# Optimization experiments

Hardware: AMD Instinct MI355X
Metric: run time of the kernel (lower is better)

## Reference

```python
import jax, jax.numpy as jnp
import numpy as np
from jax.scipy.special import logsumexp

V, E, H, T, L = 100000, 300, 512, 24, 4096


def _lstm_dir(x, w_ih, w_hh, b, reverse):
    # x: [L, Din] -> hs: [L, H]; PyTorch gate order i, f, g, o
    if reverse:
        x = x[::-1]
    pre = x @ w_ih.T + b  # [L, 4H], input projection hoisted out of scan

    def step(carry, zt):
        h, c = carry
        z = zt + h @ w_hh.T
        i, f, g, o = jnp.split(z, 4)
        i, f, o = jax.nn.sigmoid(i), jax.nn.sigmoid(f), jax.nn.sigmoid(o)
        c = f * c + i * jnp.tanh(g)
        h = o * jnp.tanh(c)
        return (h, c), h

    z0 = (jnp.zeros(H, x.dtype), jnp.zeros(H, x.dtype))
    _, hs = jax.lax.scan(step, z0, pre)
    if reverse:
        hs = hs[::-1]
    return hs


def _crf_nll(emissions, tags, start_trans, end_trans, trans):
    # emissions: [L, T], tags: [L] int. Returns -log p(tags | emissions).
    n = emissions.shape[0]
    num = (start_trans[tags[0]]
           + emissions[jnp.arange(n), tags].sum()
           + trans[tags[:-1], tags[1:]].sum()
           + end_trans[tags[-1]])

    def step(alpha, e_t):
        alpha = logsumexp(alpha[:, None] + trans, axis=0) + e_t
        return alpha, None

    alpha0 = start_trans + emissions[0]
    alpha, _ = jax.lax.scan(step, alpha0, emissions[1:])
    den = logsumexp(alpha + end_trans)
    return den - num


def setup_inputs() -> dict:
    key = jax.random.key(0)
    ks = jax.random.split(key, 24)
    s = 0.05
    inp = {
        'emb': jax.random.normal(ks[0], (V, E), jnp.float32),
        'w_ih_l0f': s * jax.random.normal(ks[1], (4 * H, E), jnp.float32),
        'w_hh_l0f': s * jax.random.normal(ks[2], (4 * H, H), jnp.float32),
        'b_l0f': s * jax.random.normal(ks[3], (4 * H,), jnp.float32),
        'w_ih_l0b': s * jax.random.normal(ks[4], (4 * H, E), jnp.float32),
        'w_hh_l0b': s * jax.random.normal(ks[5], (4 * H, H), jnp.float32),
        'b_l0b': s * jax.random.normal(ks[6], (4 * H,), jnp.float32),
        'w_ih_l1f': s * jax.random.normal(ks[7], (4 * H, 2 * H), jnp.float32),
        'w_hh_l1f': s * jax.random.normal(ks[8], (4 * H, H), jnp.float32),
        'b_l1f': s * jax.random.normal(ks[9], (4 * H,), jnp.float32),
        'w_ih_l1b': s * jax.random.normal(ks[10], (4 * H, 2 * H), jnp.float32),
        'w_hh_l1b': s * jax.random.normal(ks[11], (4 * H, H), jnp.float32),
        'b_l1b': s * jax.random.normal(ks[12], (4 * H,), jnp.float32),
        'w_out': s * jax.random.normal(ks[13], (T, 2 * H), jnp.float32),
        'b_out': s * jax.random.normal(ks[14], (T,), jnp.float32),
        'start_trans': 0.1 * jax.random.normal(ks[15], (T,), jnp.float32),
        'end_trans': 0.1 * jax.random.normal(ks[16], (T,), jnp.float32),
        'trans': 0.1 * jax.random.normal(ks[17], (T, T), jnp.float32),
        'sentence': jax.random.randint(ks[18], (L,), 0, V, jnp.int64 if jax.config.jax_enable_x64 else jnp.int32),
        'tags': jax.random.randint(ks[19], (L,), 0, T, jnp.int64 if jax.config.jax_enable_x64 else jnp.int32),
    }
    return inp


def reference(emb, w_ih_l0f, w_hh_l0f, b_l0f, w_ih_l0b, w_hh_l0b, b_l0b,
              w_ih_l1f, w_hh_l1f, b_l1f, w_ih_l1b, w_hh_l1b, b_l1b,
              w_out, b_out, start_trans, end_trans, trans, sentence, tags):
    x = emb[sentence]  # [L, E]
    # layer 0 bidirectional
    hf = _lstm_dir(x, w_ih_l0f, w_hh_l0f, b_l0f, False)
    hb = _lstm_dir(x, w_ih_l0b, w_hh_l0b, b_l0b, True)
    x = jnp.concatenate([hf, hb], axis=-1)  # [L, 2H]
    # layer 1 bidirectional
    hf = _lstm_dir(x, w_ih_l1f, w_hh_l1f, b_l1f, False)
    hb = _lstm_dir(x, w_ih_l1b, w_hh_l1b, b_l1b, True)
    x = jnp.concatenate([hf, hb], axis=-1)
    emissions = x @ w_out.T + b_out  # [L, T]
    # module returns -1 * CRF log-likelihood
    return _crf_nll(emissions, tags, start_trans, end_trans, trans)
```

## Files before the change

### kernel.cpp

```cpp
#include <hip/hip_runtime.h>

#define RK 32
#define RTH 1024
#define UPS 16
#define SEQ 4096
#define HID 512
#define NT 24

__device__ __forceinline__ float sigf(float x) { return 1.f / (1.f + __expf(-x)); }
__device__ __forceinline__ float tanhfast(float x) {
    const float e = __expf(2.f * x);
    return 1.f - 2.f / (e + 1.f);
}

__device__ __forceinline__ float4 load_f4_cc(const float* p) {
    float4 v;
    asm volatile("global_load_dwordx4 %0, %1, off sc0 sc1\n\ts_waitcnt vmcnt(0)"
                 : "=v"(v) : "v"(p) : "memory");
    return v;
}

__global__ __launch_bounds__(64)
void init_gather(const float* __restrict__ emb, const int* __restrict__ sent,
                 float* __restrict__ X0)
{
    const int b = blockIdx.x, tid = threadIdx.x;
    const size_t row = (size_t)sent[b] * 300;
    for (int e = tid; e < 300; e += 64)
        X0[(size_t)b * 300 + e] = emb[row + e];
}

__global__ __launch_bounds__(256)
void sgemm_bias(const float* __restrict__ A, const float* __restrict__ W,
                const float* __restrict__ bias, float* __restrict__ C,
                int M, int N, int K)
{
    __shared__ float As[8][128];
    __shared__ float Ws[8][128];
    const int tid = threadIdx.x;
    const int m0 = blockIdx.y * 128, n0 = blockIdx.x * 128;
    const int tx = tid & 15, ty = tid >> 4;
    const int lr = tid >> 1, lk = (tid & 1) * 4;
    float acc[8][8] = {};
    for (int k0 = 0; k0 < K; k0 += 8) {
#pragma unroll
        for (int u = 0; u < 4; ++u) {
            const int k = k0 + lk + u;
            As[lk + u][lr] = (k < K) ? A[(size_t)(m0 + lr) * K + k] : 0.f;
            Ws[lk + u][lr] = (k < K) ? W[(size_t)(n0 + lr) * K + k] : 0.f;
        }
        __syncthreads();
#pragma unroll
        for (int kk = 0; kk < 8; ++kk) {
            float a[8], b[8];
#pragma unroll
            for (int i = 0; i < 8; ++i) a[i] = As[kk][ty * 8 + i];
#pragma unroll
            for (int i = 0; i < 8; ++i) b[i] = Ws[kk][tx * 8 + i];
#pragma unroll
            for (int i = 0; i < 8; ++i)
#pragma unroll
                for (int j = 0; j < 8; ++j) acc[i][j] += a[i] * b[j];
        }
        __syncthreads();
    }
#pragma unroll
    for (int i = 0; i < 8; ++i) {
        const int m = m0 + ty * 8 + i;
#pragma unroll
        for (int j = 0; j < 8; ++j) {
            const int n = n0 + tx * 8 + j;
            C[(size_t)m * N + n] = acc[i][j] + bias[n];
        }
    }
}

__global__ __launch_bounds__(RTH, 1)
void lstm_rec(const float* __restrict__ pre_f, const float* __restrict__ pre_b,
              const float* __restrict__ whh_f, const float* __restrict__ whh_b,
              float* __restrict__ out,
              float* __restrict__ hbuf)
{
    const int g = blockIdx.x;
    const int dir = g & 1, slot = g >> 1;
    const float* pre = dir ? pre_b : pre_f;
    const float* whh = dir ? whh_b : whh_f;
    float* hb0 = hbuf + dir * 2 * HID;

    const int tid = threadIdx.x;
    const int seg = tid >> 5;
    const int rsub = tid & 31;

    const int k0g = rsub >> 4, j0 = rsub & 15;
    const int grow0 = k0g * HID + slot * UPS + j0;
    const int grow1 = (k0g + 2) * HID + slot * UPS + j0;

    float4 w0[4], w1[4];
    {
        const float4* p0 = (const float4*)(whh + (size_t)grow0 * HID + seg * 16);
        const float4* p1 = (const float4*)(whh + (size_t)grow1 * HID + seg * 16);
#pragma unroll
        for (int c = 0; c < 4; ++c) { w0[c] = p0[c]; w1[c] = p1[c]; }
    }

    const int rr = tid & 63;
    const int growr = (rr >> 4) * HID + slot * UPS + (rr & 15);

    __shared__ float h_sm[HID];
    __shared__ float zz[64][33];
    float c_state = 0.f;

    if (tid < HID) h_sm[tid] = 0.f;
    __syncthreads();

    float pre_v = 0.f;
    if (tid < 64) pre_v = pre[(size_t)(dir ? (SEQ - 1) : 0) * 2048 + growr];

    for (int t = 0; t < SEQ; ++t) {
        const int tt = dir ? (SEQ - 1 - t) : t;
        const bool not_last = (t + 1 < SEQ);

        asm volatile("" : "+v"(w0[0].x), "+v"(w0[0].y), "+v"(w0[0].z), "+v"(w0[0].w),
                           "+v"(w0[1].x), "+v"(w0[1].y), "+v"(w0[1].z), "+v"(w0[1].w),
                           "+v"(w0[2].x), "+v"(w0[2].y), "+v"(w0[2].z), "+v"(w0[2].w),
                           "+v"(w0[3].x), "+v"(w0[3].y), "+v"(w0[3].z), "+v"(w0[3].w));
        asm volatile("" : "+v"(w1[0].x), "+v"(w1[0].y), "+v"(w1[0].z), "+v"(w1[0].w),
                           "+v"(w1[1].x), "+v"(w1[1].y), "+v"(w1[1].z), "+v"(w1[1].w),
                           "+v"(w1[2].x), "+v"(w1[2].y), "+v"(w1[2].z), "+v"(w1[2].w),
                           "+v"(w1[3].x), "+v"(w1[3].y), "+v"(w1[3].z), "+v"(w1[3].w));

        const float4* hp = (const float4*)(h_sm + seg * 16);
        const float4 h0 = hp[0], h1 = hp[1], h2 = hp[2], h3 = hp[3];
        float a0, a1;
        {
            a0  = w0[0].x*h0.x + w0[0].y*h0.y + w0[0].z*h0.z + w0[0].w*h0.w;
            a0 += w0[1].x*h1.x + w0[1].y*h1.y + w0[1].z*h1.z + w0[1].w*h1.w;
            a0 += w0[2].x*h2.x + w0[2].y*h2.y + w0[2].z*h2.z + w0[2].w*h2.w;
            a0 += w0[3].x*h3.x + w0[3].y*h3.y + w0[3].z*h3.z + w0[3].w*h3.w;
            a1  = w1[0].x*h0.x + w1[0].y*h0.y + w1[0].z*h0.z + w1[0].w*h0.w;
            a1 += w1[1].x*h1.x + w1[1].y*h1.y + w1[1].z*h1.z + w1[1].w*h1.w;
            a1 += w1[2].x*h2.x + w1[2].y*h2.y + w1[2].z*h2.z + w1[2].w*h2.w;
            a1 += w1[3].x*h3.x + w1[3].y*h3.y + w1[3].z*h3.z + w1[3].w*h3.w;
        }
        zz[rsub][seg] = a0;
        zz[rsub + 32][seg] = a1;
        __syncthreads();

        float pre_next = 0.f;
        if (tid < 64 && not_last) {
            const int tn = dir ? (SEQ - 2 - t) : (t + 1);
            pre_next = pre[(size_t)tn * 2048 + growr];
        }

        if (tid < 64) {
            float s = pre_v;
#pragma unroll
            for (int c = 0; c < 32; ++c) s += zz[tid][c];
            const int lj = tid & 15;
            const float zi = __shfl(s, lj, 64);
            const float zf = __shfl(s, lj + 16, 64);
            const float zg = __shfl(s, lj + 32, 64);
            const float zo = __shfl(s, lj + 48, 64);
            if (tid < UPS) {
                const float ig = sigf(zi), fg = sigf(zf), og = sigf(zo);
                c_state = fg * c_state + ig * tanhfast(zg);
                const float h = og * tanhfast(c_state);
                out[(size_t)tt * 1024 + dir * HID + slot * UPS + lj] = h;
                if (not_last) {
                    const float off = 3.f + 6.f * (float)((t >> 1) & 1);
                    __hip_atomic_store(hb0 + (t & 1) * HID + slot * UPS + lj, h + off,
                                       __ATOMIC_RELAXED, __HIP_MEMORY_SCOPE_AGENT);
                }
            }
        }

        if (not_last) {
            if (tid < 128) {
                const float lo = 2.f + 6.f * (float)((t >> 1) & 1);
                const float hi = lo + 2.f;
                const float mid = lo + 1.f;
                const float* src = hb0 + (t & 1) * HID + tid * 4;
                float4 v;
                for (;;) {
                    v = load_f4_cc(src);
                    if (v.x >= lo && v.x <= hi && v.y >= lo && v.y <= hi &&
                        v.z >= lo && v.z <= hi && v.w >= lo && v.w <= hi) break;
                }
                float4* dst = (float4*)(h_sm + tid * 4);
                *dst = make_float4(v.x - mid, v.y - mid, v.z - mid, v.w - mid);
            }
            __syncthreads();
        }
        pre_v = pre_next;
    }
}

__global__ __launch_bounds__(256)
void emissions_kernel(const float* __restrict__ X, const float* __restrict__ Wo,
                      const float* __restrict__ bo, float* __restrict__ EM)
{
    __shared__ float xs[1024];
    __shared__ float red[NT][9];
    const int t = blockIdx.x, tid = threadIdx.x;
    for (int i = tid; i < 1024; i += 256) xs[i] = X[(size_t)t * 1024 + i];
    __syncthreads();
    const int col = tid >> 3, s = tid & 7;
    if (col < NT) {
        float acc = 0.f;
        const float* wr = Wo + (size_t)col * 1024 + s * 128;
        const float* xp = xs + s * 128;
#pragma unroll 8
        for (int i = 0; i < 128; ++i) acc += wr[i] * xp[i];
        red[col][s] = acc;
    }
    __syncthreads();
    if (tid < NT) {
        float rsum = 0.f;
#pragma unroll
        for (int s2 = 0; s2 < 8; ++s2) rsum += red[tid][s2];
        EM[t * NT + tid] = rsum + bo[tid];
    }
}

__global__ __launch_bounds__(256)
void num_kernel(const float* __restrict__ EM, const int* __restrict__ tags,
                const float* __restrict__ stt, const float* __restrict__ ent,
                const float* __restrict__ tr, float* __restrict__ numout)
{
    __shared__ float red[256];
    const int tid = threadIdx.x;
    float acc = 0.f;
    for (int t = tid; t < SEQ; t += 256) {
        const int tg = tags[t];
        acc += EM[t * NT + tg];
        if (t < SEQ - 1) acc += tr[tg * NT + tags[t + 1]];
    }
    red[tid] = acc; __syncthreads();
    for (int s = 128; s > 0; s >>= 1) { if (tid < s) red[tid] += red[tid + s]; __syncthreads(); }
    if (tid == 0) numout[0] = red[0] + stt[tags[0]] + ent[tags[SEQ - 1]];
}

__global__ __launch_bounds__(576)
void crf_stage1(const float* __restrict__ EM, const float* __restrict__ trans,
                float* __restrict__ CH)
{
    __shared__ float tr[NT][NT];
    __shared__ float cur[2][NT][NT + 1];
    const int tid = threadIdx.x;
    const int i = tid / NT, j = tid % NT;
    const int c = blockIdx.x;
    const int t0 = 1 + c * 16;
    const int cm = min(16, SEQ - t0);
    const float trv = trans[i * NT + j];
    tr[i][j] = trv;
    cur[0][i][j] = trv + EM[t0 * NT + j];
    __syncthreads();
    int pp = 0;
    for (int s = 1; s < cm; ++s) {
        const float e = EM[(t0 + s) * NT + j];
        float m = -1e30f;
#pragma unroll
        for (int k = 0; k < NT; ++k) m = fmaxf(m, cur[pp][i][k] + tr[k][j]);
        float sum = 0.f;
#pragma unroll
        for (int k = 0; k < NT; ++k) sum += __expf(cur[pp][i][k] + tr[k][j] - m);
        cur[1 - pp][i][j] = m + __logf(sum) + e;
        pp = 1 - pp;
        __syncthreads();
    }
    CH[(size_t)c * 576 + i * NT + j] = cur[pp][i][j];
}

__global__ __launch_bounds__(576)
void crf_combine(const float* __restrict__ IN, float* __restrict__ OUT, int per)
{
    __shared__ float cur[2][NT][NT + 1];
    const int tid = threadIdx.x;
    const int i = tid / NT, j = tid % NT;
    const int c = blockIdx.x;
    const float* base = IN + (size_t)c * per * 576;
    cur[0][i][j] = base[i * NT + j];
    __syncthreads();
    int pp = 0;
    for (int s = 1; s < per; ++s) {
        const float* B = base + (size_t)s * 576;
        float m = -1e30f;
#pragma unroll
        for (int k = 0; k < NT; ++k) m = fmaxf(m, cur[pp][i][k] + B[k * NT + j]);
        float sum = 0.f;
#pragma unroll
        for (int k = 0; k < NT; ++k) sum += __expf(cur[pp][i][k] + B[k * NT + j] - m);
        cur[1 - pp][i][j] = m + __logf(sum);
        pp = 1 - pp;
        __syncthreads();
    }
    OUT[(size_t)c * 576 + i * NT + j] = cur[pp][i][j];
}

__global__ __launch_bounds__(576)
void crf_final(const float* __restrict__ P2, const float* __restrict__ EM,
               const float* __restrict__ stt, const float* __restrict__ ent,
               const float* __restrict__ numptr, float* __restrict__ outp)
{
    __shared__ float cur[2][NT][NT + 1];
    __shared__ float red[1024];
    const int tid = threadIdx.x;
    const int i = tid / NT, j = tid % NT;
    cur[0][i][j] = P2[i * NT + j];
    __syncthreads();
    int pp = 0;
    for (int s = 1; s < 16; ++s) {
        const float* B = P2 + (size_t)s * 576;
        float m = -1e30f;
#pragma unroll
        for (int k = 0; k < NT; ++k) m = fmaxf(m, cur[pp][i][k] + B[k * NT + j]);
        float sum = 0.f;
#pragma unroll
        for (int k = 0; k < NT; ++k) sum += __expf(cur[pp][i][k] + B[k * NT + j] - m);
        cur[1 - pp][i][j] = m + __logf(sum);
        pp = 1 - pp;
        __syncthreads();
    }
    const float v = stt[i] + EM[i] + cur[pp][i][j] + ent[j];
    red[tid] = v;
    for (int t2 = tid + 576; t2 < 1024; t2 += 576) red[t2] = -1e30f;
    __syncthreads();
    for (int s2 = 512; s2 > 0; s2 >>= 1) {
        if (tid < s2) red[tid] = fmaxf(red[tid], red[tid + s2]);
        __syncthreads();
    }
    const float m = red[0];
    __syncthreads();
    red[tid] = __expf(v - m);
    for (int t2 = tid + 576; t2 < 1024; t2 += 576) red[t2] = 0.f;
    __syncthreads();
    for (int s2 = 512; s2 > 0; s2 >>= 1) {
        if (tid < s2) red[tid] += red[tid + s2];
        __syncthreads();
    }
    if (tid == 0) outp[0] = m + __logf(red[0]) - numptr[0];
}

extern "C" void kernel_launch(void* const* d_in, const int* in_sizes, int n_in,
                              void* d_out, int out_size, void* d_ws, size_t ws_size,
                              hipStream_t stream)
{
    const float* emb    = (const float*)d_in[0];
    const float* wih0f  = (const float*)d_in[1];
    const float* whh0f  = (const float*)d_in[2];
    const float* b0f    = (const float*)d_in[3];
    const float* wih0b  = (const float*)d_in[4];
    const float* whh0b  = (const float*)d_in[5];
    const float* b0b    = (const float*)d_in[6];
    const float* wih1f  = (const float*)d_in[7];
    const float* whh1f  = (const float*)d_in[8];
    const float* b1f    = (const float*)d_in[9];
    const float* wih1b  = (const float*)d_in[10];
    const float* whh1b  = (const float*)d_in[11];
    const float* b1b    = (const float*)d_in[12];
    const float* wout   = (const float*)d_in[13];
    const float* bout   = (const float*)d_in[14];
    const float* sttr   = (const float*)d_in[15];
    const float* entr   = (const float*)d_in[16];
    const float* trans  = (const float*)d_in[17];
    const int*   sent   = (const int*)d_in[18];
    const int*   tags   = (const int*)d_in[19];

    float* ws = (float*)d_ws;
    float* X0   = ws;
    float* PRE  = X0 + 1228800;
    float* X1   = PRE + 16777216;
    float* X2   = X1 + 4194304;
    float* EMb  = X2 + 4194304;
    float* CH   = EMb + 98304;
    float* P2   = CH + 147456;
    float* NUMv = P2 + 9216;
    float* HBUF = NUMv + 64;

    const int PREST = 8388608;

    init_gather<<<4096, 64, 0, stream>>>(emb, sent, X0);

    dim3 gg(16, 32);
    sgemm_bias<<<gg, 256, 0, stream>>>(X0, wih0f, b0f, PRE,         4096, 2048, 300);
    sgemm_bias<<<gg, 256, 0, stream>>>(X0, wih0b, b0b, PRE + PREST, 4096, 2048, 300);
    lstm_rec<<<2 * RK, RTH, 0, stream>>>(PRE, PRE + PREST, whh0f, whh0b, X1, HBUF);

    sgemm_bias<<<gg, 256, 0, stream>>>(X1, wih1f, b1f, PRE,         4096, 2048, 1024);
    sgemm_bias<<<gg, 256, 0, stream>>>(X1, wih1b, b1b, PRE + PREST, 4096, 2048, 1024);
    lstm_rec<<<2 * RK, RTH, 0, stream>>>(PRE, PRE + PREST, whh1f, whh1b, X2, HBUF + 2048);

    emissions_kernel<<<4096, 256, 0, stream>>>(X2, wout, bout, EMb);
    num_kernel<<<1, 256, 0, stream>>>(EMb, tags, sttr, entr, trans, NUMv);
    crf_stage1<<<256, 576, 0, stream>>>(EMb, trans, CH);
    crf_combine<<<16, 576, 0, stream>>>(CH, P2, 16);
    crf_final<<<1, 576, 0, stream>>>(P2, EMb, sttr, entr, NUMv, (float*)d_out);
}
```

Before: 15.57 ms.

## Poll hidden state directly into registers and drop the per-step shared-memory barrier

Each thread now polls the global hidden-state exchange buffer itself, reading its 16 h values straight into registers. This replaces the stage in which 128 threads copied h into shared memory behind an extra __syncthreads. The zz reduction buffer is double-buffered so one barrier per step suffices. An adaptive s_sleep backoff cuts polling pressure on memory. The cost is more concurrent coherent loads per step and a risk of latency added by the sleep.

Measured after the change: 20.88 ms. +34.1%, slower.

```diff
diff --git a/kernel.cpp b/kernel.cpp
--- a/kernel.cpp
+++ b/kernel.cpp
@@ -13,11 +13,21 @@
     return 1.f - 2.f / (e + 1.f);
 }
 
-__device__ __forceinline__ float4 load_f4_cc(const float* p) {
-    float4 v;
-    asm volatile("global_load_dwordx4 %0, %1, off sc0 sc1\n\ts_waitcnt vmcnt(0)"
-                 : "=v"(v) : "v"(p) : "memory");
-    return v;
+__device__ __forceinline__ bool ok4(const float4& v, float lo, float hi) {
+    return v.x >= lo && v.x <= hi && v.y >= lo && v.y <= hi &&
+           v.z >= lo && v.z <= hi && v.w >= lo && v.w <= hi;
+}
+
+__device__ __forceinline__ void load_line_cc(const float* p, float4& a, float4& b,
+                                             float4& c, float4& d) {
+    asm volatile(
+        "global_load_dwordx4 %0, %4, off sc0 sc1\n\t"
+        "global_load_dwordx4 %1, %4, off offset:16 sc0 sc1\n\t"
+        "global_load_dwordx4 %2, %4, off offset:32 sc0 sc1\n\t"
+        "global_load_dwordx4 %3, %4, off offset:48 sc0 sc1\n\t"
+        "s_waitcnt vmcnt(0)"
+        : "=v"(a), "=v"(b), "=v"(c), "=v"(d)
+        : "v"(p) : "memory");
 }
 
 __global__ __launch_bounds__(64)
@@ -106,12 +116,9 @@
     const int rr = tid & 63;
     const int growr = (rr >> 4) * HID + slot * UPS + (rr & 15);
 
-    __shared__ float h_sm[HID];
-    __shared__ float zz[64][33];
+    __shared__ float zz[2][64][33];
     float c_state = 0.f;
-
-    if (tid < HID) h_sm[tid] = 0.f;
-    __syncthreads();
+    int slp = 3;
 
     float pre_v = 0.f;
     if (tid < 64) pre_v = pre[(size_t)(dir ? (SEQ - 1) : 0) * 2048 + growr];
@@ -129,8 +136,33 @@
                            "+v"(w1[2].x), "+v"(w1[2].y), "+v"(w1[2].z), "+v"(w1[2].w),
                            "+v"(w1[3].x), "+v"(w1[3].y), "+v"(w1[3].z), "+v"(w1[3].w));
 
-        const float4* hp = (const float4*)(h_sm + seg * 16);
-        const float4 h0 = hp[0], h1 = hp[1], h2 = hp[2], h3 = hp[3];
+        float4 h0, h1, h2, h3;
+        if (t > 0) {
+            const int tp = t - 1;
+            const float lo = 2.f + 6.f * (float)((tp >> 1) & 1);
+            const float hi = lo + 2.f;
+            const float mid = lo + 1.f;
+            const float* src = hb0 + (tp & 1) * HID + seg * 16;
+            for (int sl = 0; sl < slp; ++sl) __builtin_amdgcn_s_sleep(2);
+            int misses = 0;
+            for (;;) {
+                load_line_cc(src, h0, h1, h2, h3);
+                if (ok4(h0, lo, hi) && ok4(h1, lo, hi) &&
+                    ok4(h2, lo, hi) && ok4(h3, lo, hi)) break;
+                ++misses;
+            }
+            h0.x -= mid; h0.y -= mid; h0.z -= mid; h0.w -= mid;
+            h1.x -= mid; h1.y -= mid; h1.z -= mid; h1.w -= mid;
+            h2.x -= mid; h2.y -= mid; h2.z -= mid; h2.w -= mid;
+            h3.x -= mid; h3.y -= mid; h3.z -= mid; h3.w -= mid;
+            const unsigned long long anymiss = __ballot(misses > 0);
+            if (anymiss != 0ull) { if (slp < 12) ++slp; }
+            else if ((t & 15) == 1 && slp > 0) --slp;
+        } else {
+            h0 = make_float4(0.f, 0.f, 0.f, 0.f);
+            h1 = h0; h2 = h0; h3 = h0;
+        }
+
         float a0, a1;
         {
             a0  = w0[0].x*h0.x + w0[0].y*h0.y + w0[0].z*h0.z + w0[0].w*h0.w;
@@ -142,8 +174,9 @@
             a1 += w1[2].x*h2.x + w1[2].y*h2.y + w1[2].z*h2.z + w1[2].w*h2.w;
             a1 += w1[3].x*h3.x + w1[3].y*h3.y + w1[3].z*h3.z + w1[3].w*h3.w;
         }
-        zz[rsub][seg] = a0;
-        zz[rsub + 32][seg] = a1;
+        const int zb = t & 1;
+        zz[zb][rsub][seg] = a0;
+        zz[zb][rsub + 32][seg] = a1;
         __syncthreads();
 
         float pre_next = 0.f;
@@ -155,7 +188,7 @@
         if (tid < 64) {
             float s = pre_v;
 #pragma unroll
-            for (int c = 0; c < 32; ++c) s += zz[tid][c];
+            for (int c = 0; c < 32; ++c) s += zz[zb][tid][c];
             const int lj = tid & 15;
             const float zi = __shfl(s, lj, 64);
             const float zf = __shfl(s, lj + 16, 64);
@@ -172,24 +205,6 @@
                                        __ATOMIC_RELAXED, __HIP_MEMORY_SCOPE_AGENT);
                 }
             }
-        }
-
-        if (not_last) {
-            if (tid < 128) {
-                const float lo = 2.f + 6.f * (float)((t >> 1) & 1);
-                const float hi = lo + 2.f;
-                const float mid = lo + 1.f;
-                const float* src = hb0 + (t & 1) * HID + tid * 4;
-                float4 v;
-                for (;;) {
-                    v = load_f4_cc(src);
-                    if (v.x >= lo && v.x <= hi && v.y >= lo && v.y <= hi &&
-                        v.z >= lo && v.z <= hi && v.w >= lo && v.w <= hi) break;
-                }
-                float4* dst = (float4*)(h_sm + tid * 4);
-                *dst = make_float4(v.x - mid, v.y - mid, v.z - mid, v.w - mid);
-            }
-            __syncthreads();
         }
         pre_v = pre_next;
     }
```
